# Optimization experiments

Hardware: AMD Instinct MI355X
Metric: run time of the kernel (lower is better)

## Reference

```python
import jax, jax.numpy as jnp
import numpy as np

N_GRAPHS = 100
NODES_PER_GRAPH = 1000
N = N_GRAPHS * NODES_PER_GRAPH
DEG = 16
E = N * DEG
IN_FEATS = 64
HIDDEN = 128
READOUT_DIM = HIDDEN // 2
SLOPE = 0.01
EPS = 1e-5


def leaky(x):
    return jnp.where(x >= 0, x, SLOPE * x)


def _kaiming(k, shape):
    # torch kaiming_uniform_, fan_in mode, leaky_relu gain
    fan_in = shape[0]
    gain = np.sqrt(2.0 / (1.0 + SLOPE ** 2))
    bound = gain * np.sqrt(3.0 / fan_in)
    return jax.random.uniform(k, shape, jnp.float32, -bound, bound)


def setup_inputs() -> dict:
    key = jax.random.key(0)
    ks = jax.random.split(key, 16)
    node_feats = jax.random.normal(ks[0], (N, IN_FEATS), jnp.float32)
    # within-graph random edges (batched graph of equal-sized components)
    src_local = jax.random.randint(ks[1], (E,), 0, NODES_PER_GRAPH)
    dst_local = jax.random.randint(ks[2], (E,), 0, NODES_PER_GRAPH)
    edge_graph = jnp.repeat(jnp.arange(N_GRAPHS, dtype=jnp.int32), E // N_GRAPHS)
    src = (edge_graph * NODES_PER_GRAPH + src_local).astype(jnp.int32)
    dst = (edge_graph * NODES_PER_GRAPH + dst_local).astype(jnp.int32)
    edge_weights = jax.random.uniform(ks[3], (E,), jnp.float32)
    node_graph = jnp.repeat(jnp.arange(N_GRAPHS, dtype=jnp.int32), NODES_PER_GRAPH)
    return {
        "node_feats": node_feats,
        "edge_weights": edge_weights,
        "W1": _kaiming(ks[4], (IN_FEATS, HIDDEN)),
        "W2": _kaiming(ks[5], (HIDDEN, HIDDEN)),
        "gn1_alpha": jnp.ones((HIDDEN,), jnp.float32),
        "gn1_gamma": jnp.ones((HIDDEN,), jnp.float32),
        "gn1_beta": jnp.zeros((HIDDEN,), jnp.float32),
        "gn2_alpha": jnp.ones((HIDDEN,), jnp.float32),
        "gn2_gamma": jnp.ones((HIDDEN,), jnp.float32),
        "gn2_beta": jnp.zeros((HIDDEN,), jnp.float32),
        "r1_w1": _kaiming(ks[6], (HIDDEN, HIDDEN)),
        "r1_b1": jnp.zeros((HIDDEN,), jnp.float32),
        "r1_w2": _kaiming(ks[7], (HIDDEN, READOUT_DIM)),
        "r1_b2": jnp.zeros((READOUT_DIM,), jnp.float32),
        "r2_w1": _kaiming(ks[8], (HIDDEN, HIDDEN)),
        "r2_b1": jnp.zeros((HIDDEN,), jnp.float32),
        "r2_w2": _kaiming(ks[9], (HIDDEN, READOUT_DIM)),
        "r2_b2": jnp.zeros((READOUT_DIM,), jnp.float32),
        "src": src,
        "dst": dst,
        "node_graph": node_graph,
    }


def _graph_conv(x, W, src, dst, ew, out_isqrt, in_isqrt):
    # DGL GraphConv norm='both', no bias: D_in^{-1/2} A_w D_out^{-1/2} X W
    h = (x * out_isqrt[:, None]) @ W                 # [N, out]
    m = h[src] * ew[:, None]                         # [E, out] gather + edge weight
    agg = jax.ops.segment_sum(m, dst, num_segments=N)  # scatter-add
    return agg * in_isqrt[:, None]


def _graph_norm(x, alpha, gamma, beta, node_graph, inv_cnt):
    mean = jax.ops.segment_sum(x, node_graph, num_segments=N_GRAPHS) * inv_cnt
    sub = x - alpha * mean[node_graph]
    var = jax.ops.segment_sum(sub * sub, node_graph, num_segments=N_GRAPHS) * inv_cnt
    return gamma * sub / jnp.sqrt(var[node_graph] + EPS) + beta


def _readout(x, w1, b1, w2, b2, node_graph, inv_cnt):
    # deep-sets style universal readout: rho(mean(phi(h_v)))
    h = leaky(x @ w1 + b1)
    pooled = jax.ops.segment_sum(h, node_graph, num_segments=N_GRAPHS) * inv_cnt
    return leaky(pooled @ w2 + b2)


def reference(node_feats, edge_weights, W1, W2,
              gn1_alpha, gn1_gamma, gn1_beta,
              gn2_alpha, gn2_gamma, gn2_beta,
              r1_w1, r1_b1, r1_w2, r1_b2,
              r2_w1, r2_b1, r2_w2, r2_b2,
              src, dst, node_graph):
    ones_e = jnp.ones((E,), jnp.float32)
    out_deg = jnp.clip(jax.ops.segment_sum(ones_e, src, num_segments=N), 1.0)
    in_deg = jnp.clip(jax.ops.segment_sum(ones_e, dst, num_segments=N), 1.0)
    out_isqrt = jax.lax.rsqrt(out_deg)
    in_isqrt = jax.lax.rsqrt(in_deg)
    inv_cnt = 1.0 / NODES_PER_GRAPH

    h = _graph_conv(node_feats, W1, src, dst, edge_weights, out_isqrt, in_isqrt)
    h = leaky(_graph_norm(h, gn1_alpha, gn1_gamma, gn1_beta, node_graph, inv_cnt))
    # dropout is identity in eval mode
    r1 = _readout(h, r1_w1, r1_b1, r1_w2, r1_b2, node_graph, inv_cnt)
    m1 = jax.ops.segment_sum(h, node_graph, num_segments=N_GRAPHS) * inv_cnt

    h = _graph_conv(h, W2, src, dst, edge_weights, out_isqrt, in_isqrt)
    h = leaky(_graph_norm(h, gn2_alpha, gn2_gamma, gn2_beta, node_graph, inv_cnt))
    r2 = _readout(h, r2_w1, r2_b1, r2_w2, r2_b2, node_graph, inv_cnt)
    m2 = jax.ops.segment_sum(h, node_graph, num_segments=N_GRAPHS) * inv_cnt

    readout = jnp.concatenate([r1, m1, r2, m2], axis=1)  # [G, 2*H + 2*H/2] = [100, 384]
    return leaky(readout)
```

## Files before the change

### kernel.cpp

```cpp
#include <hip/hip_runtime.h>
#include <cstddef>
#include <cstdint>

#define NG   100
#define NPG  1000
#define NN   (NG * NPG)
#define NE   (NN * 16)
#define EPG  (NE / NG)
#define CSRG 20000
#define FIN  64
#define HID  128
#define RD   64
#define SLOPE 0.01f
#define EPSV  1e-5f
#define NSTRIP 250
#define GSN   40

using short8 = __attribute__((ext_vector_type(8))) short;
using f32x4  = __attribute__((ext_vector_type(4))) float;
typedef unsigned short u16;

__device__ __forceinline__ float leaky(float x) { return x >= 0.f ? x : SLOPE * x; }

__device__ __forceinline__ u16 f2bf(float f) {
  union { float f; unsigned u; } v; v.f = f;
  return (u16)((v.u + 0x7fffu + ((v.u >> 16) & 1u)) >> 16);
}
__device__ __forceinline__ float bf2f(u16 u) {
  union { unsigned u; float f; } v; v.u = ((unsigned)u) << 16;
  return v.f;
}

__device__ __forceinline__ bool swz(int b, int per_g, int& g, int& part) {
  const int xcd = b & 7;
  const int slot = b >> 3;
  g = xcd + 8 * (slot / per_g);
  part = slot % per_g;
  return g < NG;
}

__global__ __launch_bounds__(256) void wt_k(const float* __restrict__ W1,
                                            const float* __restrict__ W2,
                                            const float* __restrict__ R1,
                                            const float* __restrict__ R2,
                                            u16* __restrict__ Wt1,
                                            u16* __restrict__ Wt2,
                                            u16* __restrict__ Rt1,
                                            u16* __restrict__ Rt2) {
  const int idx = blockIdx.x * 256 + threadIdx.x;
  if (idx < FIN * HID) {
    const int n = idx >> 6, k = idx & 63;
    Wt1[idx] = f2bf(W1[k * HID + n]);
  } else {
    const int j = idx - FIN * HID;
    const int m = j >> 14, r = j & 16383;
    const int n = r >> 7, k = r & 127;
    const float* s = (m == 0) ? W2 : (m == 1) ? R1 : R2;
    u16* d = (m == 0) ? Wt2 : (m == 1) ? Rt1 : Rt2;
    d[r] = f2bf(s[k * HID + n]);
  }
}

__global__ __launch_bounds__(1024) void build_k(const int* __restrict__ src,
                                                const int* __restrict__ dst,
                                                const float* __restrict__ ew,
                                                int* __restrict__ cin_,
                                                int* __restrict__ cout_,
                                                int* __restrict__ offs,
                                                unsigned* __restrict__ csr) {
  __shared__ int hin[NPG];
  __shared__ int hout[NPG];
  __shared__ int cur[NPG];
  __shared__ int wtot[16];
  int g, part;
  if (!swz(blockIdx.x, 1, g, part)) return;
  const int t = threadIdx.x;
  const int lane = t & 63, wave = t >> 6;
  const int nb = g * NPG, eb = g * EPG;
  if (t < NPG) { hin[t] = 0; hout[t] = 0; }
  __syncthreads();
  for (int e = t; e < EPG; e += 4096) {
    int s4[4], d4[4];
#pragma unroll
    for (int k = 0; k < 4; ++k) {
      const int ee = e + k * 1024;
      if (ee < EPG) { s4[k] = src[eb + ee]; d4[k] = dst[eb + ee]; }
      else d4[k] = -1;
    }
#pragma unroll
    for (int k = 0; k < 4; ++k)
      if (d4[k] >= 0) {
        atomicAdd(&hout[s4[k] - nb], 1);
        atomicAdd(&hin[d4[k] - nb], 1);
      }
  }
  __syncthreads();
  int v[4], vr[4];
  int loc = 0;
#pragma unroll
  for (int k = 0; k < 4; ++k) {
    const int idx = t * 4 + k;
    v[k] = (idx < NPG) ? hin[idx] : 0;
    vr[k] = (v[k] + 3) & ~3;
    loc += vr[k];
  }
  int incl = loc;
#pragma unroll
  for (int d = 1; d < 64; d <<= 1) {
    const int x = __shfl_up(incl, d);
    if (lane >= d) incl += x;
  }
  if (lane == 63) wtot[wave] = incl;
  if (t < NPG) { cin_[nb + t] = hin[t]; cout_[nb + t] = hout[t]; }
  __syncthreads();
  int wexc = 0;
  for (int i = 0; i < wave; ++i) wexc += wtot[i];
  int run = g * CSRG + wexc + (incl - loc);
#pragma unroll
  for (int k = 0; k < 4; ++k) {
    const int idx = t * 4 + k;
    if (idx < NPG) {
      offs[nb + idx] = run;
      cur[idx] = run;
      run += vr[k];
    }
  }
  __syncthreads();
  for (int e = t; e < EPG; e += 4096) {
    int s4[4], d4[4]; float w4[4];
#pragma unroll
    for (int k = 0; k < 4; ++k) {
      const int ee = e + k * 1024;
      if (ee < EPG) { s4[k] = src[eb + ee]; d4[k] = dst[eb + ee]; w4[k] = ew[eb + ee]; }
      else d4[k] = -1;
    }
#pragma unroll
    for (int k = 0; k < 4; ++k)
      if (d4[k] >= 0) {
        const int pos = atomicAdd(&cur[d4[k] - nb], 1);
        csr[pos] = ((unsigned)(s4[k] - nb) << 16) | (unsigned)f2bf(w4[k]);
      }
  }
}

__global__ __launch_bounds__(256) void gemm1_k(const float* __restrict__ X,
                                               const u16* __restrict__ Wt,
                                               const int* __restrict__ cout_,
                                               u16* __restrict__ Y) {
  __shared__ u16 Xl[64 * FIN];
  __shared__ u16 Wl[HID * FIN];
  const int tid = threadIdx.x;
  const int wave = tid >> 6, lane = tid & 63, l15 = lane & 15, quad = lane >> 4;
  int g, part;
  if (!swz(blockIdx.x, 4, g, part)) return;
  const int base = g * NPG + part * NSTRIP;
  const int kq = tid & 15;
  const int srow = tid >> 4;

  for (int i = tid; i < HID * (FIN / 8); i += 256) {
    const int n = i >> 3, c = i & 7;
    const short8 w = *(const short8*)(Wt + n * FIN + c * 8);
    *(short8*)&Wl[n * FIN + ((c ^ (n & 7)) << 3)] = w;
  }
  float4 xpre[4];
#pragma unroll
  for (int it = 0; it < 4; ++it) {
    const int rowi = srow + it * 16;
    xpre[it] = (rowi < NSTRIP) ? *(const float4*)(X + (size_t)(base + rowi) * FIN + kq * 4)
                               : make_float4(0.f, 0.f, 0.f, 0.f);
  }
  for (int pass = 0; pass < 4; ++pass) {
    __syncthreads();
#pragma unroll
    for (int it = 0; it < 4; ++it) {
      const int r = srow + it * 16;
      ushort4 u = make_ushort4(f2bf(xpre[it].x), f2bf(xpre[it].y),
                               f2bf(xpre[it].z), f2bf(xpre[it].w));
      const int c = kq >> 1, half = kq & 1;
      *(ushort4*)&Xl[r * FIN + (((c ^ (r & 7)) << 3) | (half << 2))] = u;
    }
    __syncthreads();
    if (pass < 3) {
#pragma unroll
      for (int it = 0; it < 4; ++it) {
        const int rowi = (pass + 1) * 64 + srow + it * 16;
        xpre[it] = (rowi < NSTRIP) ? *(const float4*)(X + (size_t)(base + rowi) * FIN + kq * 4)
                                   : make_float4(0.f, 0.f, 0.f, 0.f);
      }
    }
    short8 a[2];
    const int arow = wave * 16 + l15;
#pragma unroll
    for (int kt = 0; kt < 2; ++kt)
      a[kt] = *(const short8*)&Xl[arow * FIN + (((kt * 4 + quad) ^ (l15 & 7)) << 3)];
    float sc[4];
    int rows[4];
#pragma unroll
    for (int r = 0; r < 4; ++r) {
      rows[r] = pass * 64 + wave * 16 + quad * 4 + r;
      sc[r] = (rows[r] < NSTRIP) ? rsqrtf(fmaxf((float)cout_[base + rows[r]], 1.0f)) : 0.f;
    }
#pragma unroll
    for (int ct = 0; ct < 8; ++ct) {
      f32x4 acc = {0.f, 0.f, 0.f, 0.f};
      const int brow = ct * 16 + l15;
#pragma unroll
      for (int kt = 0; kt < 2; ++kt) {
        const short8 b = *(const short8*)&Wl[brow * FIN + (((kt * 4 + quad) ^ (l15 & 7)) << 3)];
        acc = __builtin_amdgcn_mfma_f32_16x16x32_bf16(a[kt], b, acc, 0, 0, 0);
      }
      const int n = ct * 16 + l15;
#pragma unroll
      for (int r = 0; r < 4; ++r)
        if (rows[r] < NSTRIP) Y[(size_t)(base + rows[r]) * HID + n] = f2bf(acc[r] * sc[r]);
    }
  }
}

__global__ __launch_bounds__(256) void gemm_norm_k(const u16* __restrict__ Xb,
                                                   const u16* __restrict__ Wt,
                                                   const float* __restrict__ An,
                                                   const float* __restrict__ Bn,
                                                   const int* __restrict__ cout_,
                                                   u16* __restrict__ Y) {
  __shared__ u16 Xl[64 * HID];
  __shared__ u16 Wl[HID * HID];
  const int tid = threadIdx.x;
  const int wave = tid >> 6, lane = tid & 63, l15 = lane & 15, quad = lane >> 4;
  int g, part;
  if (!swz(blockIdx.x, 4, g, part)) return;
  const int base = g * NPG + part * NSTRIP;
  const int c8 = tid & 15;
  const int srow = tid >> 4;

  for (int i = tid; i < HID * (HID / 8); i += 256) {
    const int n = i >> 4, c = i & 15;
    const short8 w = *(const short8*)(Wt + n * HID + c * 8);
    *(short8*)&Wl[n * HID + ((c ^ (n & 15)) << 3)] = w;
  }
  float Av[8], Bv[8];
  {
    const float4 Aa = *(const float4*)(An + (size_t)g * HID + c8 * 8);
    const float4 Ab = *(const float4*)(An + (size_t)g * HID + c8 * 8 + 4);
    const float4 Ba = *(const float4*)(Bn + (size_t)g * HID + c8 * 8);
    const float4 Bb = *(const float4*)(Bn + (size_t)g * HID + c8 * 8 + 4);
    Av[0] = Aa.x; Av[1] = Aa.y; Av[2] = Aa.z; Av[3] = Aa.w;
    Av[4] = Ab.x; Av[5] = Ab.y; Av[6] = Ab.z; Av[7] = Ab.w;
    Bv[0] = Ba.x; Bv[1] = Ba.y; Bv[2] = Ba.z; Bv[3] = Ba.w;
    Bv[4] = Bb.x; Bv[5] = Bb.y; Bv[6] = Bb.z; Bv[7] = Bb.w;
  }
  const short8 z8 = {0, 0, 0, 0, 0, 0, 0, 0};
  short8 xpre[4];
#pragma unroll
  for (int it = 0; it < 4; ++it) {
    const int rowi = srow + it * 16;
    xpre[it] = (rowi < NSTRIP) ? *(const short8*)(Xb + (size_t)(base + rowi) * HID + c8 * 8) : z8;
  }
  for (int pass = 0; pass < 4; ++pass) {
    __syncthreads();
#pragma unroll
    for (int it = 0; it < 4; ++it) {
      const int r = srow + it * 16;
      const int rowi = pass * 64 + r;
      short8 o = z8;
      if (rowi < NSTRIP) {
#pragma unroll
        for (int j = 0; j < 8; ++j)
          o[j] = (short)f2bf(leaky(fmaf(Av[j], bf2f((u16)xpre[it][j]), Bv[j])));
      }
      *(short8*)&Xl[r * HID + ((c8 ^ (r & 15)) << 3)] = o;
    }
    __syncthreads();
    if (pass < 3) {
#pragma unroll
      for (int it = 0; it < 4; ++it) {
        const int rowi = (pass + 1) * 64 + srow + it * 16;
        xpre[it] = (rowi < NSTRIP) ? *(const short8*)(Xb + (size_t)(base + rowi) * HID + c8 * 8) : z8;
      }
    }
    short8 a[4];
    const int arow = wave * 16 + l15;
#pragma unroll
    for (int kt = 0; kt < 4; ++kt)
      a[kt] = *(const short8*)&Xl[arow * HID + (((kt * 4 + quad) ^ l15) << 3)];
    float sc[4];
    int rows[4];
#pragma unroll
    for (int r = 0; r < 4; ++r) {
      rows[r] = pass * 64 + wave * 16 + quad * 4 + r;
      sc[r] = (rows[r] < NSTRIP) ? rsqrtf(fmaxf((float)cout_[base + rows[r]], 1.0f)) : 0.f;
    }
#pragma unroll
    for (int ct = 0; ct < 8; ++ct) {
      f32x4 acc = {0.f, 0.f, 0.f, 0.f};
      const int brow = ct * 16 + l15;
#pragma unroll
      for (int kt = 0; kt < 4; ++kt) {
        const short8 b = *(const short8*)&Wl[brow * HID + (((kt * 4 + quad) ^ l15) << 3)];
        acc = __builtin_amdgcn_mfma_f32_16x16x32_bf16(a[kt], b, acc, 0, 0, 0);
      }
      const int n = ct * 16 + l15;
#pragma unroll
      for (int r = 0; r < 4; ++r)
        if (rows[r] < NSTRIP) Y[(size_t)(base + rows[r]) * HID + n] = f2bf(acc[r] * sc[r]);
    }
  }
}

struct RedT { float red[16][HID]; float hred[16][HID]; };
union ShT { u16 Xl[64 * HID]; RedT r; };

__global__ __launch_bounds__(256) void phi_pool_k(const u16* __restrict__ Xb,
                                                  const float* __restrict__ An,
                                                  const float* __restrict__ Bn,
                                                  const u16* __restrict__ Wt,
                                                  const float* __restrict__ b1,
                                                  float* __restrict__ phi_sum,
                                                  float* __restrict__ h_sum) {
  __shared__ ShT sh;
  __shared__ u16 Wl[HID * HID];
  const int tid = threadIdx.x;
  const int wave = tid >> 6, lane = tid & 63, l15 = lane & 15, quad = lane >> 4;
  int g, part;
  if (!swz(blockIdx.x, 4, g, part)) return;
  const int base = g * NPG + part * NSTRIP;
  const int c8 = tid & 15;
  const int srow = tid >> 4;

  for (int i = tid; i < HID * (HID / 8); i += 256) {
    const int n = i >> 4, c = i & 15;
    const short8 w = *(const short8*)(Wt + n * HID + c * 8);
    *(short8*)&Wl[n * HID + ((c ^ (n & 15)) << 3)] = w;
  }
  float Av[8], Bv[8];
  {
    const float4 Aa = *(const float4*)(An + (size_t)g * HID + c8 * 8);
    const float4 Ab = *(const float4*)(An + (size_t)g * HID + c8 * 8 + 4);
    const float4 Ba = *(const float4*)(Bn + (size_t)g * HID + c8 * 8);
    const float4 Bb = *(const float4*)(Bn + (size_t)g * HID + c8 * 8 + 4);
    Av[0] = Aa.x; Av[1] = Aa.y; Av[2] = Aa.z; Av[3] = Aa.w;
    Av[4] = Ab.x; Av[5] = Ab.y; Av[6] = Ab.z; Av[7] = Ab.w;
    Bv[0] = Ba.x; Bv[1] = Ba.y; Bv[2] = Ba.z; Bv[3] = Ba.w;
    Bv[4] = Bb.x; Bv[5] = Bb.y; Bv[6] = Bb.z; Bv[7] = Bb.w;
  }
  float bcol[8];
#pragma unroll
  for (int ct = 0; ct < 8; ++ct) bcol[ct] = b1[ct * 16 + l15];

  float pooled[8] = {0.f, 0.f, 0.f, 0.f, 0.f, 0.f, 0.f, 0.f};
  float hp[8] = {0.f, 0.f, 0.f, 0.f, 0.f, 0.f, 0.f, 0.f};
  const short8 z8 = {0, 0, 0, 0, 0, 0, 0, 0};
  short8 xpre[4];
#pragma unroll
  for (int it = 0; it < 4; ++it) {
    const int rowi = srow + it * 16;
    xpre[it] = (rowi < NSTRIP) ? *(const short8*)(Xb + (size_t)(base + rowi) * HID + c8 * 8) : z8;
  }
  for (int pass = 0; pass < 4; ++pass) {
    __syncthreads();
#pragma unroll
    for (int it = 0; it < 4; ++it) {
      const int r = srow + it * 16;
      const int rowi = pass * 64 + r;
      short8 o = z8;
      if (rowi < NSTRIP) {
#pragma unroll
        for (int j = 0; j < 8; ++j) {
          const float xn = leaky(fmaf(Av[j], bf2f((u16)xpre[it][j]), Bv[j]));
          hp[j] += xn;
          o[j] = (short)f2bf(xn);
        }
      }
      *(short8*)&sh.Xl[r * HID + ((c8 ^ (r & 15)) << 3)] = o;
    }
    __syncthreads();
    if (pass < 3) {
#pragma unroll
      for (int it = 0; it < 4; ++it) {
        const int rowi = (pass + 1) * 64 + srow + it * 16;
        xpre[it] = (rowi < NSTRIP) ? *(const short8*)(Xb + (size_t)(base + rowi) * HID + c8 * 8) : z8;
      }
    }
    short8 a[4];
    const int arow = wave * 16 + l15;
#pragma unroll
    for (int kt = 0; kt < 4; ++kt)
      a[kt] = *(const short8*)&sh.Xl[arow * HID + (((kt * 4 + quad) ^ l15) << 3)];
#pragma unroll
    for (int ct = 0; ct < 8; ++ct) {
      f32x4 acc = {0.f, 0.f, 0.f, 0.f};
      const int brow = ct * 16 + l15;
#pragma unroll
      for (int kt = 0; kt < 4; ++kt) {
        const short8 b = *(const short8*)&Wl[brow * HID + (((kt * 4 + quad) ^ l15) << 3)];
        acc = __builtin_amdgcn_mfma_f32_16x16x32_bf16(a[kt], b, acc, 0, 0, 0);
      }
#pragma unroll
      for (int r = 0; r < 4; ++r) {
        const int rowi = pass * 64 + wave * 16 + quad * 4 + r;
        if (rowi < NSTRIP) pooled[ct] += leaky(acc[r] + bcol[ct]);
      }
    }
  }
  __syncthreads();
  const int qi = wave * 4 + quad;
#pragma unroll
  for (int ct = 0; ct < 8; ++ct) sh.r.red[qi][ct * 16 + l15] = pooled[ct];
#pragma unroll
  for (int j = 0; j < 8; ++j) sh.r.hred[tid >> 4][(tid & 15) * 8 + j] = hp[j];
  __syncthreads();
  if (tid < HID) {
    float s = 0.f;
#pragma unroll
    for (int q = 0; q < 16; ++q) s += sh.r.red[q][tid];
    unsafeAtomicAdd(&phi_sum[g * HID + tid], s);
  } else {
    const int t = tid - HID;
    float s = 0.f;
#pragma unroll
    for (int rr = 0; rr < 16; ++rr) s += sh.r.hred[rr][t];
    unsafeAtomicAdd(&h_sum[g * HID + t], s);
  }
}

__global__ __launch_bounds__(256) void gather_k(const u16* __restrict__ H,
                                                const unsigned* __restrict__ csr,
                                                const int* __restrict__ offs,
                                                const int* __restrict__ cin_,
                                                u16* __restrict__ AGG,
                                                float* __restrict__ sx,
                                                float* __restrict__ sq) {
  __shared__ float redx[4][HID];
  __shared__ float redq[4][HID];
  const int wave = threadIdx.x >> 6;
  const int lane = threadIdx.x & 63;
  int g, part;
  if (!swz(blockIdx.x, 25, g, part)) return;
  const int nb = g * NPG;
  const int base = nb + part * GSN;
  const int loff = lane * 2;
  const u16* __restrict__ Hg = H + (size_t)nb * HID;

  float sxa = 0.f, sxb = 0.f, sqa = 0.f, sqb = 0.f;
  for (int i = 0; i < 5; ++i) {
    const int nA = base + wave + i * 4;
    const int nB = nA + GSN / 2;
    const int nuA = __builtin_amdgcn_readfirstlane(nA);
    const int nuB = __builtin_amdgcn_readfirstlane(nB);
    const int offA = __builtin_amdgcn_readfirstlane(offs[nuA]);
    const int cntA = __builtin_amdgcn_readfirstlane(cin_[nuA]);
    const int offB = __builtin_amdgcn_readfirstlane(offs[nuB]);
    const int cntB = __builtin_amdgcn_readfirstlane(cin_[nuB]);
    const float isqA = rsqrtf(fmaxf((float)cntA, 1.0f));
    const float isqB = rsqrtf(fmaxf((float)cntB, 1.0f));
    const uint4* __restrict__ pA =
        (const uint4*)__builtin_assume_aligned(csr + offA, 16);
    const uint4* __restrict__ pB =
        (const uint4*)__builtin_assume_aligned(csr + offB, 16);
    float axA = 0.f, ayA = 0.f, bxA = 0.f, byA = 0.f;
    float axB = 0.f, ayB = 0.f, bxB = 0.f, byB = 0.f;
    const int c4A = cntA >> 2, c4B = cntB >> 2;
    const int common = min(c4A, c4B);
    int t = 0;
    for (; t < common; ++t) {
      const uint4 rA = pA[t];
      const uint4 rB = pB[t];
      const unsigned a0 = *(const unsigned*)(Hg + (size_t)(rA.x >> 16) * HID + loff);
      const unsigned a1 = *(const unsigned*)(Hg + (size_t)(rA.y >> 16) * HID + loff);
      const unsigned a2 = *(const unsigned*)(Hg + (size_t)(rA.z >> 16) * HID + loff);
      const unsigned a3 = *(const unsigned*)(Hg + (size_t)(rA.w >> 16) * HID + loff);
      const unsigned b0 = *(const unsigned*)(Hg + (size_t)(rB.x >> 16) * HID + loff);
      const unsigned b1 = *(const unsigned*)(Hg + (size_t)(rB.y >> 16) * HID + loff);
      const unsigned b2 = *(const unsigned*)(Hg + (size_t)(rB.z >> 16) * HID + loff);
      const unsigned b3 = *(const unsigned*)(Hg + (size_t)(rB.w >> 16) * HID + loff);
      const float wA0 = bf2f((u16)(rA.x & 0xffffu));
      const float wA1 = bf2f((u16)(rA.y & 0xffffu));
      const float wA2 = bf2f((u16)(rA.z & 0xffffu));
      const float wA3 = bf2f((u16)(rA.w & 0xffffu));
      const float wB0 = bf2f((u16)(rB.x & 0xffffu));
      const float wB1 = bf2f((u16)(rB.y & 0xffffu));
      const float wB2 = bf2f((u16)(rB.z & 0xffffu));
      const float wB3 = bf2f((u16)(rB.w & 0xffffu));
      axA = fmaf(wA0, __uint_as_float(a0 << 16), axA);
      ayA = fmaf(wA0, __uint_as_float(a0 & 0xffff0000u), ayA);
      bxA = fmaf(wA1, __uint_as_float(a1 << 16), bxA);
      byA = fmaf(wA1, __uint_as_float(a1 & 0xffff0000u), byA);
      axA = fmaf(wA2, __uint_as_float(a2 << 16), axA);
      ayA = fmaf(wA2, __uint_as_float(a2 & 0xffff0000u), ayA);
      bxA = fmaf(wA3, __uint_as_float(a3 << 16), bxA);
      byA = fmaf(wA3, __uint_as_float(a3 & 0xffff0000u), byA);
      axB = fmaf(wB0, __uint_as_float(b0 << 16), axB);
      ayB = fmaf(wB0, __uint_as_float(b0 & 0xffff0000u), ayB);
      bxB = fmaf(wB1, __uint_as_float(b1 << 16), bxB);
      byB = fmaf(wB1, __uint_as_float(b1 & 0xffff0000u), byB);
      axB = fmaf(wB2, __uint_as_float(b2 << 16), axB);
      ayB = fmaf(wB2, __uint_as_float(b2 & 0xffff0000u), ayB);
      bxB = fmaf(wB3, __uint_as_float(b3 << 16), bxB);
      byB = fmaf(wB3, __uint_as_float(b3 & 0xffff0000u), byB);
    }
    for (int ta = t; ta < c4A; ++ta) {
      const uint4 rA = pA[ta];
      const unsigned a0 = *(const unsigned*)(Hg + (size_t)(rA.x >> 16) * HID + loff);
      const unsigned a1 = *(const unsigned*)(Hg + (size_t)(rA.y >> 16) * HID + loff);
      const unsigned a2 = *(const unsigned*)(Hg + (size_t)(rA.z >> 16) * HID + loff);
      const unsigned a3 = *(const unsigned*)(Hg + (size_t)(rA.w >> 16) * HID + loff);
      const float w0 = bf2f((u16)(rA.x & 0xffffu));
      const float w1 = bf2f((u16)(rA.y & 0xffffu));
      const float w2 = bf2f((u16)(rA.z & 0xffffu));
      const float w3 = bf2f((u16)(rA.w & 0xffffu));
      axA = fmaf(w0, __uint_as_float(a0 << 16), axA);
      ayA = fmaf(w0, __uint_as_float(a0 & 0xffff0000u), ayA);
      bxA = fmaf(w1, __uint_as_float(a1 << 16), bxA);
      byA = fmaf(w1, __uint_as_float(a1 & 0xffff0000u), byA);
      axA = fmaf(w2, __uint_as_float(a2 << 16), axA);
      ayA = fmaf(w2, __uint_as_float(a2 & 0xffff0000u), ayA);
      bxA = fmaf(w3, __uint_as_float(a3 << 16), bxA);
      byA = fmaf(w3, __uint_as_float(a3 & 0xffff0000u), byA);
    }
    for (int tb = t; tb < c4B; ++tb) {
      const uint4 rB = pB[tb];
      const unsigned b0 = *(const unsigned*)(Hg + (size_t)(rB.x >> 16) * HID + loff);
      const unsigned b1 = *(const unsigned*)(Hg + (size_t)(rB.y >> 16) * HID + loff);
      const unsigned b2 = *(const unsigned*)(Hg + (size_t)(rB.z >> 16) * HID + loff);
      const unsigned b3 = *(const unsigned*)(Hg + (size_t)(rB.w >> 16) * HID + loff);
      const float w0 = bf2f((u16)(rB.x & 0xffffu));
      const float w1 = bf2f((u16)(rB.y & 0xffffu));
      const float w2 = bf2f((u16)(rB.z & 0xffffu));
      const float w3 = bf2f((u16)(rB.w & 0xffffu));
      axB = fmaf(w0, __uint_as_float(b0 << 16), axB);
      ayB = fmaf(w0, __uint_as_float(b0 & 0xffff0000u), ayB);
      bxB = fmaf(w1, __uint_as_float(b1 << 16), bxB);
      byB = fmaf(w1, __uint_as_float(b1 & 0xffff0000u), byB);
      axB = fmaf(w2, __uint_as_float(b2 << 16), axB);
      ayB = fmaf(w2, __uint_as_float(b2 & 0xffff0000u), ayB);
      bxB = fmaf(w3, __uint_as_float(b3 << 16), bxB);
      byB = fmaf(w3, __uint_as_float(b3 & 0xffff0000u), byB);
    }
    for (int k = c4A << 2; k < cntA; ++k) {
      const unsigned r0 = csr[offA + k];
      const float w = bf2f((u16)(r0 & 0xffffu));
      const unsigned u0 = *(const unsigned*)(Hg + (size_t)(r0 >> 16) * HID + loff);
      axA = fmaf(w, __uint_as_float(u0 << 16), axA);
      ayA = fmaf(w, __uint_as_float(u0 & 0xffff0000u), ayA);
    }
    for (int k = c4B << 2; k < cntB; ++k) {
      const unsigned r0 = csr[offB + k];
      const float w = bf2f((u16)(r0 & 0xffffu));
      const unsigned u0 = *(const unsigned*)(Hg + (size_t)(r0 >> 16) * HID + loff);
      axB = fmaf(w, __uint_as_float(u0 << 16), axB);
      ayB = fmaf(w, __uint_as_float(u0 & 0xffff0000u), ayB);
    }
    const float rxA = (axA + bxA) * isqA;
    const float ryA = (ayA + byA) * isqA;
    const float rxB = (axB + bxB) * isqB;
    const float ryB = (ayB + byB) * isqB;
    *(unsigned*)(AGG + (size_t)nA * HID + loff) =
        (unsigned)f2bf(rxA) | ((unsigned)f2bf(ryA) << 16);
    *(unsigned*)(AGG + (size_t)nB * HID + loff) =
        (unsigned)f2bf(rxB) | ((unsigned)f2bf(ryB) << 16);
    sxa += rxA + rxB; sxb += ryA + ryB;
    sqa += rxA * rxA + rxB * rxB;
    sqb += ryA * ryA + ryB * ryB;
  }
  redx[wave][loff] = sxa; redx[wave][loff + 1] = sxb;
  redq[wave][loff] = sqa; redq[wave][loff + 1] = sqb;
  __syncthreads();
  const int tid = threadIdx.x;
  if (tid < HID) {
    unsafeAtomicAdd(&sx[g * HID + tid],
                    redx[0][tid] + redx[1][tid] + redx[2][tid] + redx[3][tid]);
  } else {
    const int t = tid - HID;
    unsafeAtomicAdd(&sq[g * HID + t],
                    redq[0][t] + redq[1][t] + redq[2][t] + redq[3][t]);
  }
}

__global__ __launch_bounds__(HID) void stats_k(const float* __restrict__ sx,
                                               const float* __restrict__ sq,
                                               const float* __restrict__ alpha,
                                               const float* __restrict__ gamma,
                                               const float* __restrict__ beta,
                                               float* __restrict__ An,
                                               float* __restrict__ Bn) {
  const int g = (blockIdx.x & 7) + 8 * (blockIdx.x >> 3);
  if (g >= NG) return;
  const int j = threadIdx.x;
  const float mean = sx[g * HID + j] * (1.0f / NPG);
  const float ex2 = sq[g * HID + j] * (1.0f / NPG);
  const float am = alpha[j] * mean;
  float var = ex2 - 2.0f * am * mean + am * am;
  var = fmaxf(var, 0.0f);
  const float rstd = rsqrtf(var + EPSV);
  const float A = gamma[j] * rstd;
  An[g * HID + j] = A;
  Bn[g * HID + j] = beta[j] - A * am;
}

__global__ __launch_bounds__(64) void finalize_k(const float* __restrict__ phi_sum,
                                                 const float* __restrict__ h_sum,
                                                 const float* __restrict__ w2,
                                                 const float* __restrict__ b2,
                                                 float* __restrict__ out,
                                                 int roff, int moff) {
  const int g = blockIdx.x;
  const int j = threadIdx.x;
  float acc = b2[j];
#pragma unroll 8
  for (int k = 0; k < HID; ++k)
    acc += (phi_sum[g * HID + k] * (1.0f / NPG)) * w2[k * RD + j];
  const float r = leaky(acc);
  out[g * 384 + roff + j] = leaky(r);
  out[g * 384 + moff + j] = leaky(h_sum[g * HID + j] * (1.0f / NPG));
  out[g * 384 + moff + 64 + j] = leaky(h_sum[g * HID + 64 + j] * (1.0f / NPG));
}

extern "C" void kernel_launch(void* const* d_in, const int* in_sizes, int n_in,
                              void* d_out, int out_size, void* d_ws, size_t ws_size,
                              hipStream_t stream) {
  const float* node_feats = (const float*)d_in[0];
  const float* ew   = (const float*)d_in[1];
  const float* W1   = (const float*)d_in[2];
  const float* W2   = (const float*)d_in[3];
  const float* g1a  = (const float*)d_in[4];
  const float* g1g  = (const float*)d_in[5];
  const float* g1b  = (const float*)d_in[6];
  const float* g2a  = (const float*)d_in[7];
  const float* g2g  = (const float*)d_in[8];
  const float* g2b  = (const float*)d_in[9];
  const float* r1w1 = (const float*)d_in[10];
  const float* r1b1 = (const float*)d_in[11];
  const float* r1w2 = (const float*)d_in[12];
  const float* r1b2 = (const float*)d_in[13];
  const float* r2w1 = (const float*)d_in[14];
  const float* r2b1 = (const float*)d_in[15];
  const float* r2w2 = (const float*)d_in[16];
  const float* r2b2 = (const float*)d_in[17];
  const int* src = (const int*)d_in[18];
  const int* dst = (const int*)d_in[19];
  float* out = (float*)d_out;

  char* wsb = (char*)d_ws;
  float* ps1     = (float*)wsb;
  float* hs1     = ps1 + NG * HID;
  float* ps2     = hs1 + NG * HID;
  float* hs2     = ps2 + NG * HID;
  float* sx1     = hs2 + NG * HID;
  float* sq1     = sx1 + NG * HID;
  float* sx2     = sq1 + NG * HID;
  float* sq2     = sx2 + NG * HID;
  int*   cin     = (int*)(sq2 + NG * HID);
  int*   cout_   = cin + NN;
  int*   offs    = cout_ + NN;
  unsigned* csr  = (unsigned*)(offs + NN);
  float* A1      = (float*)(csr + (size_t)NG * CSRG);
  float* B1      = A1 + NG * HID;
  float* A2      = B1 + NG * HID;
  float* B2      = A2 + NG * HID;
  u16*   Wt1     = (u16*)(B2 + NG * HID);
  u16*   Wt2     = Wt1 + HID * FIN;
  u16*   Rt1     = Wt2 + HID * HID;
  u16*   Rt2     = Rt1 + HID * HID;
  u16*   bufA    = Rt2 + HID * HID;
  u16*   bufB    = bufA + (size_t)NN * HID;

  hipMemsetAsync(d_ws, 0, (size_t)(8 * NG * HID) * sizeof(float), stream);

  wt_k<<<(FIN * HID + 3 * HID * HID) / 256, 256, 0, stream>>>(
      W1, W2, r1w1, r2w1, Wt1, Wt2, Rt1, Rt2);
  build_k<<<8 * 13, 1024, 0, stream>>>(src, dst, ew, cin, cout_, offs, csr);

  const int gemm_grid = 8 * 4 * 13;
  const int gather_grid = 8 * 25 * 13;
  const int stats_grid = 8 * 13;

  gemm1_k<<<gemm_grid, 256, 0, stream>>>(node_feats, Wt1, cout_, bufA);
  gather_k<<<gather_grid, 256, 0, stream>>>(bufA, csr, offs, cin, bufB, sx1, sq1);
  stats_k<<<stats_grid, HID, 0, stream>>>(sx1, sq1, g1a, g1g, g1b, A1, B1);
  phi_pool_k<<<gemm_grid, 256, 0, stream>>>(bufB, A1, B1, Rt1, r1b1, ps1, hs1);
  finalize_k<<<NG, 64, 0, stream>>>(ps1, hs1, r1w2, r1b2, out, 0, 64);

  gemm_norm_k<<<gemm_grid, 256, 0, stream>>>(bufB, Wt2, A1, B1, cout_, bufA);
  gather_k<<<gather_grid, 256, 0, stream>>>(bufA, csr, offs, cin, bufB, sx2, sq2);
  stats_k<<<stats_grid, HID, 0, stream>>>(sx2, sq2, g2a, g2g, g2b, A2, B2);
  phi_pool_k<<<gemm_grid, 256, 0, stream>>>(bufB, A2, B2, Rt2, r2b1, ps2, hs2);
  finalize_k<<<NG, 64, 0, stream>>>(ps2, hs2, r2w2, r2b2, out, 192, 256);
}
```

Measured before the change: 297.2 us.

## Fold graph-norm stats into consumers and gather four nodes per wave

Removes the separate stats_k launches by having phi_pool_k and gemm_norm_k compute the per-graph norm scale and shift inline from the summed statistics. The gather kernel is also restructured to process four destination nodes at once instead of two, giving more independent gather loads in flight per wave. This saves two kernel launches and their dependency bubbles in exchange for redundant per-block rsqrt work and higher register pressure in the gather loop. The wider gather also repeats the offs lookup for dummy slots in the last iteration.

Result: no change. 295.0 us (-0.8%).

```diff
diff --git a/kernel.cpp b/kernel.cpp
--- a/kernel.cpp
+++ b/kernel.cpp
@@ -217,10 +217,31 @@
   }
 }
 
+__device__ __forceinline__ void norm_affine(const float* sx, const float* sq,
+                                            const float* alpha, const float* gamma,
+                                            const float* beta, int g, int c8,
+                                            float* Av, float* Bv) {
+  const float inv = 1.0f / NPG;
+#pragma unroll
+  for (int j = 0; j < 8; ++j) {
+    const int f = c8 * 8 + j;
+    const float mean = sx[g * HID + f] * inv;
+    const float ex2 = sq[g * HID + f] * inv;
+    const float am = alpha[f] * mean;
+    const float var = fmaxf(ex2 - 2.0f * am * mean + am * am, 0.0f);
+    const float A = gamma[f] * rsqrtf(var + EPSV);
+    Av[j] = A;
+    Bv[j] = beta[f] - A * am;
+  }
+}
+
 __global__ __launch_bounds__(256) void gemm_norm_k(const u16* __restrict__ Xb,
                                                    const u16* __restrict__ Wt,
-                                                   const float* __restrict__ An,
-                                                   const float* __restrict__ Bn,
+                                                   const float* __restrict__ sx,
+                                                   const float* __restrict__ sq,
+                                                   const float* __restrict__ alpha,
+                                                   const float* __restrict__ gamma,
+                                                   const float* __restrict__ beta,
                                                    const int* __restrict__ cout_,
                                                    u16* __restrict__ Y) {
   __shared__ u16 Xl[64 * HID];
@@ -239,16 +260,7 @@
     *(short8*)&Wl[n * HID + ((c ^ (n & 15)) << 3)] = w;
   }
   float Av[8], Bv[8];
-  {
-    const float4 Aa = *(const float4*)(An + (size_t)g * HID + c8 * 8);
-    const float4 Ab = *(const float4*)(An + (size_t)g * HID + c8 * 8 + 4);
-    const float4 Ba = *(const float4*)(Bn + (size_t)g * HID + c8 * 8);
-    const float4 Bb = *(const float4*)(Bn + (size_t)g * HID + c8 * 8 + 4);
-    Av[0] = Aa.x; Av[1] = Aa.y; Av[2] = Aa.z; Av[3] = Aa.w;
-    Av[4] = Ab.x; Av[5] = Ab.y; Av[6] = Ab.z; Av[7] = Ab.w;
-    Bv[0] = Ba.x; Bv[1] = Ba.y; Bv[2] = Ba.z; Bv[3] = Ba.w;
-    Bv[4] = Bb.x; Bv[5] = Bb.y; Bv[6] = Bb.z; Bv[7] = Bb.w;
-  }
+  norm_affine(sx, sq, alpha, gamma, beta, g, c8, Av, Bv);
   const short8 z8 = {0, 0, 0, 0, 0, 0, 0, 0};
   short8 xpre[4];
 #pragma unroll
@@ -311,8 +323,11 @@
 union ShT { u16 Xl[64 * HID]; RedT r; };
 
 __global__ __launch_bounds__(256) void phi_pool_k(const u16* __restrict__ Xb,
-                                                  const float* __restrict__ An,
-                                                  const float* __restrict__ Bn,
+                                                  const float* __restrict__ sx,
+                                                  const float* __restrict__ sq,
+                                                  const float* __restrict__ alpha,
+                                                  const float* __restrict__ gamma,
+                                                  const float* __restrict__ beta,
                                                   const u16* __restrict__ Wt,
                                                   const float* __restrict__ b1,
                                                   float* __restrict__ phi_sum,
@@ -333,16 +348,7 @@
     *(short8*)&Wl[n * HID + ((c ^ (n & 15)) << 3)] = w;
   }
   float Av[8], Bv[8];
-  {
-    const float4 Aa = *(const float4*)(An + (size_t)g * HID + c8 * 8);
-    const float4 Ab = *(const float4*)(An + (size_t)g * HID + c8 * 8 + 4);
-    const float4 Ba = *(const float4*)(Bn + (size_t)g * HID + c8 * 8);
-    const float4 Bb = *(const float4*)(Bn + (size_t)g * HID + c8 * 8 + 4);
-    Av[0] = Aa.x; Av[1] = Aa.y; Av[2] = Aa.z; Av[3] = Aa.w;
-    Av[4] = Ab.x; Av[5] = Ab.y; Av[6] = Ab.z; Av[7] = Ab.w;
-    Bv[0] = Ba.x; Bv[1] = Ba.y; Bv[2] = Ba.z; Bv[3] = Ba.w;
-    Bv[4] = Bb.x; Bv[5] = Bb.y; Bv[6] = Bb.z; Bv[7] = Bb.w;
-  }
+  norm_affine(sx, sq, alpha, gamma, beta, g, c8, Av, Bv);
   float bcol[8];
 #pragma unroll
   for (int ct = 0; ct < 8; ++ct) bcol[ct] = b1[ct * 16 + l15];
@@ -442,125 +448,95 @@
   const u16* __restrict__ Hg = H + (size_t)nb * HID;
 
   float sxa = 0.f, sxb = 0.f, sqa = 0.f, sqb = 0.f;
-  for (int i = 0; i < 5; ++i) {
-    const int nA = base + wave + i * 4;
-    const int nB = nA + GSN / 2;
-    const int nuA = __builtin_amdgcn_readfirstlane(nA);
-    const int nuB = __builtin_amdgcn_readfirstlane(nB);
-    const int offA = __builtin_amdgcn_readfirstlane(offs[nuA]);
-    const int cntA = __builtin_amdgcn_readfirstlane(cin_[nuA]);
-    const int offB = __builtin_amdgcn_readfirstlane(offs[nuB]);
-    const int cntB = __builtin_amdgcn_readfirstlane(cin_[nuB]);
-    const float isqA = rsqrtf(fmaxf((float)cntA, 1.0f));
-    const float isqB = rsqrtf(fmaxf((float)cntB, 1.0f));
-    const uint4* __restrict__ pA =
-        (const uint4*)__builtin_assume_aligned(csr + offA, 16);
-    const uint4* __restrict__ pB =
-        (const uint4*)__builtin_assume_aligned(csr + offB, 16);
-    float axA = 0.f, ayA = 0.f, bxA = 0.f, byA = 0.f;
-    float axB = 0.f, ayB = 0.f, bxB = 0.f, byB = 0.f;
-    const int c4A = cntA >> 2, c4B = cntB >> 2;
-    const int common = min(c4A, c4B);
-    int t = 0;
-    for (; t < common; ++t) {
-      const uint4 rA = pA[t];
-      const uint4 rB = pB[t];
-      const unsigned a0 = *(const unsigned*)(Hg + (size_t)(rA.x >> 16) * HID + loff);
-      const unsigned a1 = *(const unsigned*)(Hg + (size_t)(rA.y >> 16) * HID + loff);
-      const unsigned a2 = *(const unsigned*)(Hg + (size_t)(rA.z >> 16) * HID + loff);
-      const unsigned a3 = *(const unsigned*)(Hg + (size_t)(rA.w >> 16) * HID + loff);
-      const unsigned b0 = *(const unsigned*)(Hg + (size_t)(rB.x >> 16) * HID + loff);
-      const unsigned b1 = *(const unsigned*)(Hg + (size_t)(rB.y >> 16) * HID + loff);
-      const unsigned b2 = *(const unsigned*)(Hg + (size_t)(rB.z >> 16) * HID + loff);
-      const unsigned b3 = *(const unsigned*)(Hg + (size_t)(rB.w >> 16) * HID + loff);
-      const float wA0 = bf2f((u16)(rA.x & 0xffffu));
-      const float wA1 = bf2f((u16)(rA.y & 0xffffu));
-      const float wA2 = bf2f((u16)(rA.z & 0xffffu));
-      const float wA3 = bf2f((u16)(rA.w & 0xffffu));
-      const float wB0 = bf2f((u16)(rB.x & 0xffffu));
-      const float wB1 = bf2f((u16)(rB.y & 0xffffu));
-      const float wB2 = bf2f((u16)(rB.z & 0xffffu));
-      const float wB3 = bf2f((u16)(rB.w & 0xffffu));
-      axA = fmaf(wA0, __uint_as_float(a0 << 16), axA);
-      ayA = fmaf(wA0, __uint_as_float(a0 & 0xffff0000u), ayA);
-      bxA = fmaf(wA1, __uint_as_float(a1 << 16), bxA);
-      byA = fmaf(wA1, __uint_as_float(a1 & 0xffff0000u), byA);
-      axA = fmaf(wA2, __uint_as_float(a2 << 16), axA);
-      ayA = fmaf(wA2, __uint_as_float(a2 & 0xffff0000u), ayA);
-      bxA = fmaf(wA3, __uint_as_float(a3 << 16), bxA);
-      byA = fmaf(wA3, __uint_as_float(a3 & 0xffff0000u), byA);
-      axB = fmaf(wB0, __uint_as_float(b0 << 16), axB);
-      ayB = fmaf(wB0, __uint_as_float(b0 & 0xffff0000u), ayB);
-      bxB = fmaf(wB1, __uint_as_float(b1 << 16), bxB);
-      byB = fmaf(wB1, __uint_as_float(b1 & 0xffff0000u), byB);
-      axB = fmaf(wB2, __uint_as_float(b2 << 16), axB);
-      ayB = fmaf(wB2, __uint_as_float(b2 & 0xffff0000u), ayB);
-      bxB = fmaf(wB3, __uint_as_float(b3 << 16), bxB);
-      byB = fmaf(wB3, __uint_as_float(b3 & 0xffff0000u), byB);
-    }
-    for (int ta = t; ta < c4A; ++ta) {
-      const uint4 rA = pA[ta];
-      const unsigned a0 = *(const unsigned*)(Hg + (size_t)(rA.x >> 16) * HID + loff);
-      const unsigned a1 = *(const unsigned*)(Hg + (size_t)(rA.y >> 16) * HID + loff);
-      const unsigned a2 = *(const unsigned*)(Hg + (size_t)(rA.z >> 16) * HID + loff);
-      const unsigned a3 = *(const unsigned*)(Hg + (size_t)(rA.w >> 16) * HID + loff);
-      const float w0 = bf2f((u16)(rA.x & 0xffffu));
-      const float w1 = bf2f((u16)(rA.y & 0xffffu));
-      const float w2 = bf2f((u16)(rA.z & 0xffffu));
-      const float w3 = bf2f((u16)(rA.w & 0xffffu));
-      axA = fmaf(w0, __uint_as_float(a0 << 16), axA);
-      ayA = fmaf(w0, __uint_as_float(a0 & 0xffff0000u), ayA);
-      bxA = fmaf(w1, __uint_as_float(a1 << 16), bxA);
-      byA = fmaf(w1, __uint_as_float(a1 & 0xffff0000u), byA);
-      axA = fmaf(w2, __uint_as_float(a2 << 16), axA);
-      ayA = fmaf(w2, __uint_as_float(a2 & 0xffff0000u), ayA);
-      bxA = fmaf(w3, __uint_as_float(a3 << 16), bxA);
-      byA = fmaf(w3, __uint_as_float(a3 & 0xffff0000u), byA);
-    }
-    for (int tb = t; tb < c4B; ++tb) {
-      const uint4 rB = pB[tb];
-      const unsigned b0 = *(const unsigned*)(Hg + (size_t)(rB.x >> 16) * HID + loff);
-      const unsigned b1 = *(const unsigned*)(Hg + (size_t)(rB.y >> 16) * HID + loff);
-      const unsigned b2 = *(const unsigned*)(Hg + (size_t)(rB.z >> 16) * HID + loff);
-      const unsigned b3 = *(const unsigned*)(Hg + (size_t)(rB.w >> 16) * HID + loff);
-      const float w0 = bf2f((u16)(rB.x & 0xffffu));
-      const float w1 = bf2f((u16)(rB.y & 0xffffu));
-      const float w2 = bf2f((u16)(rB.z & 0xffffu));
-      const float w3 = bf2f((u16)(rB.w & 0xffffu));
-      axB = fmaf(w0, __uint_as_float(b0 << 16), axB);
-      ayB = fmaf(w0, __uint_as_float(b0 & 0xffff0000u), ayB);
-      bxB = fmaf(w1, __uint_as_float(b1 << 16), bxB);
-      byB = fmaf(w1, __uint_as_float(b1 & 0xffff0000u), byB);
-      axB = fmaf(w2, __uint_as_float(b2 << 16), axB);
-      ayB = fmaf(w2, __uint_as_float(b2 & 0xffff0000u), ayB);
-      bxB = fmaf(w3, __uint_as_float(b3 << 16), bxB);
-      byB = fmaf(w3, __uint_as_float(b3 & 0xffff0000u), byB);
-    }
-    for (int k = c4A << 2; k < cntA; ++k) {
-      const unsigned r0 = csr[offA + k];
-      const float w = bf2f((u16)(r0 & 0xffffu));
-      const unsigned u0 = *(const unsigned*)(Hg + (size_t)(r0 >> 16) * HID + loff);
-      axA = fmaf(w, __uint_as_float(u0 << 16), axA);
-      ayA = fmaf(w, __uint_as_float(u0 & 0xffff0000u), ayA);
-    }
-    for (int k = c4B << 2; k < cntB; ++k) {
-      const unsigned r0 = csr[offB + k];
-      const float w = bf2f((u16)(r0 & 0xffffu));
-      const unsigned u0 = *(const unsigned*)(Hg + (size_t)(r0 >> 16) * HID + loff);
-      axB = fmaf(w, __uint_as_float(u0 << 16), axB);
-      ayB = fmaf(w, __uint_as_float(u0 & 0xffff0000u), ayB);
-    }
-    const float rxA = (axA + bxA) * isqA;
-    const float ryA = (ayA + byA) * isqA;
-    const float rxB = (axB + bxB) * isqB;
-    const float ryB = (ayB + byB) * isqB;
-    *(unsigned*)(AGG + (size_t)nA * HID + loff) =
-        (unsigned)f2bf(rxA) | ((unsigned)f2bf(ryA) << 16);
-    *(unsigned*)(AGG + (size_t)nB * HID + loff) =
-        (unsigned)f2bf(rxB) | ((unsigned)f2bf(ryB) << 16);
-    sxa += rxA + rxB; sxb += ryA + ryB;
-    sqa += rxA * rxA + rxB * rxB;
-    sqb += ryA * ryA + ryB * ryB;
+  for (int it = 0; it < 3; ++it) {
+    const int nc = (it < 2) ? 4 : 2;
+    int nn[4], off[4], cnt[4], c4[4];
+    float isq[4];
+    const uint4* p[4];
+#pragma unroll
+    for (int c = 0; c < 4; ++c) {
+      const int j = it * 4 + c;
+      const int node = base + wave + ((j < 10) ? j : 0) * 4;
+      nn[c] = node;
+      const int nu = __builtin_amdgcn_readfirstlane(node);
+      off[c] = __builtin_amdgcn_readfirstlane(offs[nu]);
+      cnt[c] = (c < nc) ? __builtin_amdgcn_readfirstlane(cin_[nu]) : 0;
+      c4[c] = cnt[c] >> 2;
+      isq[c] = rsqrtf(fmaxf((float)cnt[c], 1.0f));
+      p[c] = (const uint4*)__builtin_assume_aligned(csr + off[c], 16);
+    }
+    float ax[4] = {0.f, 0.f, 0.f, 0.f};
+    float ay[4] = {0.f, 0.f, 0.f, 0.f};
+    int common = min(c4[0], c4[1]);
+    if (nc == 4) common = min(common, min(c4[2], c4[3]));
+    for (int t = 0; t < common; ++t) {
+      uint4 r[4];
+      unsigned u[4][4];
+#pragma unroll
+      for (int c = 0; c < 4; ++c)
+        if (c < nc) {
+          r[c] = p[c][t];
+          u[c][0] = *(const unsigned*)(Hg + (size_t)(r[c].x >> 16) * HID + loff);
+          u[c][1] = *(const unsigned*)(Hg + (size_t)(r[c].y >> 16) * HID + loff);
+          u[c][2] = *(const unsigned*)(Hg + (size_t)(r[c].z >> 16) * HID + loff);
+          u[c][3] = *(const unsigned*)(Hg + (size_t)(r[c].w >> 16) * HID + loff);
+        }
+#pragma unroll
+      for (int c = 0; c < 4; ++c)
+        if (c < nc) {
+          const float w0 = bf2f((u16)(r[c].x & 0xffffu));
+          const float w1 = bf2f((u16)(r[c].y & 0xffffu));
+          const float w2 = bf2f((u16)(r[c].z & 0xffffu));
+          const float w3 = bf2f((u16)(r[c].w & 0xffffu));
+          ax[c] = fmaf(w0, __uint_as_float(u[c][0] << 16), ax[c]);
+          ay[c] = fmaf(w0, __uint_as_float(u[c][0] & 0xffff0000u), ay[c]);
+          ax[c] = fmaf(w1, __uint_as_float(u[c][1] << 16), ax[c]);
+          ay[c] = fmaf(w1, __uint_as_float(u[c][1] & 0xffff0000u), ay[c]);
+          ax[c] = fmaf(w2, __uint_as_float(u[c][2] << 16), ax[c]);
+          ay[c] = fmaf(w2, __uint_as_float(u[c][2] & 0xffff0000u), ay[c]);
+          ax[c] = fmaf(w3, __uint_as_float(u[c][3] << 16), ax[c]);
+          ay[c] = fmaf(w3, __uint_as_float(u[c][3] & 0xffff0000u), ay[c]);
+        }
+    }
+#pragma unroll
+    for (int c = 0; c < 4; ++c) {
+      for (int t = common; t < c4[c]; ++t) {
+        const uint4 r = p[c][t];
+        const unsigned u0 = *(const unsigned*)(Hg + (size_t)(r.x >> 16) * HID + loff);
+        const unsigned u1 = *(const unsigned*)(Hg + (size_t)(r.y >> 16) * HID + loff);
+        const unsigned u2 = *(const unsigned*)(Hg + (size_t)(r.z >> 16) * HID + loff);
+        const unsigned u3 = *(const unsigned*)(Hg + (size_t)(r.w >> 16) * HID + loff);
+        const float w0 = bf2f((u16)(r.x & 0xffffu));
+        const float w1 = bf2f((u16)(r.y & 0xffffu));
+        const float w2 = bf2f((u16)(r.z & 0xffffu));
+        const float w3 = bf2f((u16)(r.w & 0xffffu));
+        ax[c] = fmaf(w0, __uint_as_float(u0 << 16), ax[c]);
+        ay[c] = fmaf(w0, __uint_as_float(u0 & 0xffff0000u), ay[c]);
+        ax[c] = fmaf(w1, __uint_as_float(u1 << 16), ax[c]);
+        ay[c] = fmaf(w1, __uint_as_float(u1 & 0xffff0000u), ay[c]);
+        ax[c] = fmaf(w2, __uint_as_float(u2 << 16), ax[c]);
+        ay[c] = fmaf(w2, __uint_as_float(u2 & 0xffff0000u), ay[c]);
+        ax[c] = fmaf(w3, __uint_as_float(u3 << 16), ax[c]);
+        ay[c] = fmaf(w3, __uint_as_float(u3 & 0xffff0000u), ay[c]);
+      }
+      for (int k = c4[c] << 2; k < cnt[c]; ++k) {
+        const unsigned r0 = csr[off[c] + k];
+        const float w = bf2f((u16)(r0 & 0xffffu));
+        const unsigned u0 = *(const unsigned*)(Hg + (size_t)(r0 >> 16) * HID + loff);
+        ax[c] = fmaf(w, __uint_as_float(u0 << 16), ax[c]);
+        ay[c] = fmaf(w, __uint_as_float(u0 & 0xffff0000u), ay[c]);
+      }
+    }
+#pragma unroll
+    for (int c = 0; c < 4; ++c)
+      if (c < nc) {
+        const float rx = ax[c] * isq[c];
+        const float ry = ay[c] * isq[c];
+        *(unsigned*)(AGG + (size_t)nn[c] * HID + loff) =
+            (unsigned)f2bf(rx) | ((unsigned)f2bf(ry) << 16);
+        sxa += rx; sxb += ry;
+        sqa += rx * rx; sqb += ry * ry;
+      }
   }
   redx[wave][loff] = sxa; redx[wave][loff + 1] = sxb;
   redq[wave][loff] = sqa; redq[wave][loff + 1] = sqb;
@@ -574,27 +550,6 @@
     unsafeAtomicAdd(&sq[g * HID + t],
                     redq[0][t] + redq[1][t] + redq[2][t] + redq[3][t]);
   }
-}
-
-__global__ __launch_bounds__(HID) void stats_k(const float* __restrict__ sx,
-                                               const float* __restrict__ sq,
-                                               const float* __restrict__ alpha,
-                                               const float* __restrict__ gamma,
-                                               const float* __restrict__ beta,
-                                               float* __restrict__ An,
-                                               float* __restrict__ Bn) {
-  const int g = (blockIdx.x & 7) + 8 * (blockIdx.x >> 3);
-  if (g >= NG) return;
-  const int j = threadIdx.x;
-  const float mean = sx[g * HID + j] * (1.0f / NPG);
-  const float ex2 = sq[g * HID + j] * (1.0f / NPG);
-  const float am = alpha[j] * mean;
-  float var = ex2 - 2.0f * am * mean + am * am;
-  var = fmaxf(var, 0.0f);
-  const float rstd = rsqrtf(var + EPSV);
-  const float A = gamma[j] * rstd;
-  An[g * HID + j] = A;
-  Bn[g * HID + j] = beta[j] - A * am;
 }
 
 __global__ __launch_bounds__(64) void finalize_k(const float* __restrict__ phi_sum,
@@ -653,11 +608,7 @@
   int*   cout_   = cin + NN;
   int*   offs    = cout_ + NN;
   unsigned* csr  = (unsigned*)(offs + NN);
-  float* A1      = (float*)(csr + (size_t)NG * CSRG);
-  float* B1      = A1 + NG * HID;
-  float* A2      = B1 + NG * HID;
-  float* B2      = A2 + NG * HID;
-  u16*   Wt1     = (u16*)(B2 + NG * HID);
+  u16*   Wt1     = (u16*)(csr + (size_t)NG * CSRG);
   u16*   Wt2     = Wt1 + HID * FIN;
   u16*   Rt1     = Wt2 + HID * HID;
   u16*   Rt2     = Rt1 + HID * HID;
@@ -672,17 +623,17 @@
 
   const int gemm_grid = 8 * 4 * 13;
   const int gather_grid = 8 * 25 * 13;
-  const int stats_grid = 8 * 13;
 
   gemm1_k<<<gemm_grid, 256, 0, stream>>>(node_feats, Wt1, cout_, bufA);
   gather_k<<<gather_grid, 256, 0, stream>>>(bufA, csr, offs, cin, bufB, sx1, sq1);
-  stats_k<<<stats_grid, HID, 0, stream>>>(sx1, sq1, g1a, g1g, g1b, A1, B1);
-  phi_pool_k<<<gemm_grid, 256, 0, stream>>>(bufB, A1, B1, Rt1, r1b1, ps1, hs1);
+  phi_pool_k<<<gemm_grid, 256, 0, stream>>>(bufB, sx1, sq1, g1a, g1g, g1b,
+                                            Rt1, r1b1, ps1, hs1);
   finalize_k<<<NG, 64, 0, stream>>>(ps1, hs1, r1w2, r1b2, out, 0, 64);
 
-  gemm_norm_k<<<gemm_grid, 256, 0, stream>>>(bufB, Wt2, A1, B1, cout_, bufA);
+  gemm_norm_k<<<gemm_grid, 256, 0, stream>>>(bufB, Wt2, sx1, sq1, g1a, g1g, g1b,
+                                             cout_, bufA);
   gather_k<<<gather_grid, 256, 0, stream>>>(bufA, csr, offs, cin, bufB, sx2, sq2);
-  stats_k<<<stats_grid, HID, 0, stream>>>(sx2, sq2, g2a, g2g, g2b, A2, B2);
-  phi_pool_k<<<gemm_grid, 256, 0, stream>>>(bufB, A2, B2, Rt2, r2b1, ps2, hs2);
+  phi_pool_k<<<gemm_grid, 256, 0, stream>>>(bufB, sx2, sq2, g2a, g2g, g2b,
+                                            Rt2, r2b1, ps2, hs2);
   finalize_k<<<NG, 64, 0, stream>>>(ps2, hs2, r2w2, r2b2, out, 192, 256);
 }
```
